# Optimization experiments

Hardware: AMD Instinct MI355X
Metric: run time of the kernel (lower is better)

The kernel has to match this reference:

```python
import jax, jax.numpy as jnp
import numpy as np

B, C, H, W = 16, 512, 32, 32
KC = C // 8  # key_channels = 64


def setup_inputs() -> dict:
    key = jax.random.key(0)
    ks = jax.random.split(key, 6)
    s_in = 1.0 / np.sqrt(C)
    return {
        "x": jax.random.normal(ks[0], (B, C, H, W), dtype=jnp.float32),
        "Wq": jax.random.normal(ks[1], (KC, C), dtype=jnp.float32) * s_in,
        "bq": jnp.zeros((KC,), dtype=jnp.float32),
        "Wk": jax.random.normal(ks[2], (KC, C), dtype=jnp.float32) * s_in,
        "bk": jnp.zeros((KC,), dtype=jnp.float32),
        "Wv": jax.random.normal(ks[3], (C, C), dtype=jnp.float32) * s_in,
        "bv": jnp.zeros((C,), dtype=jnp.float32),
        "Wo": jax.random.normal(ks[4], (C, C), dtype=jnp.float32) * s_in,
        "bo": jnp.zeros((C,), dtype=jnp.float32),
        "gamma": jnp.zeros((1,), dtype=jnp.float32),
    }


def reference(x, Wq, bq, Wk, bk, Wv, bv, Wo, bo, gamma):
    b, c, h, w = x.shape
    n = h * w
    kc = Wq.shape[0]
    xf = x.reshape(b, c, n)  # [B, C, N]
    # 1x1 convs == channel matmuls
    q = jnp.einsum('kc,bcn->bnk', Wq, xf) + bq  # [B, N, KC]
    k = jnp.einsum('kc,bcn->bkn', Wk, xf) + bk[None, :, None]  # [B, KC, N]
    v = jnp.einsum('vc,bcn->bnv', Wv, xf) + bv  # [B, N, C]
    scale = jnp.asarray(kc, x.dtype) ** -0.5
    att = jax.nn.softmax(jnp.einsum('bnk,bkm->bnm', q, k) * scale, axis=-1)  # [B, N, N]
    out = jnp.einsum('bnm,bmv->bnv', att, v)  # [B, N, C]
    out = jnp.einsum('cv,bnv->bcn', Wo, out) + bo[None, :, None]  # [B, C, N]
    out = gamma[0] * out + xf
    return out.reshape(b, c, h, w)
```

## Files before the change

kernel.cpp:

```cpp
#include <hip/hip_runtime.h>
#include <cstddef>


typedef unsigned short ushort_t;
typedef __attribute__((ext_vector_type(8))) short bf16x8;
typedef __attribute__((ext_vector_type(4))) float f32x4;

#define QSCALE 0.18033688011112042f

__device__ __forceinline__ ushort_t f2bf_t(float f) {
  return (ushort_t)(__float_as_uint(f) >> 16);
}
__device__ __forceinline__ unsigned pk2bf(float lo, float hi) {
  return __builtin_amdgcn_perm(__float_as_uint(hi), __float_as_uint(lo),
                               0x07060302u);
}

__device__ __forceinline__ void gload16(const ushort_t* g, ushort_t* l) {
  __builtin_amdgcn_global_load_lds(
      (const __attribute__((address_space(1))) void*)g,
      (__attribute__((address_space(3))) void*)l, 16, 0, 0);
}

template <int TM>
__device__ __forceinline__ void gemm_core(
    const ushort_t* __restrict__ A, int lda,
    const ushort_t* __restrict__ B, int ldb,
    int K, int m0, int n0,
    ushort_t* As, ushort_t* Bs, f32x4 (*acc)[4])
{
  constexpr int MT  = TM / 32;
  constexpr int WTM = TM / 2;
  const int t = threadIdx.x;
  const int lane = t & 63, quad = lane >> 4, l15 = lane & 15;
  const int w = t >> 6, wm = w >> 1, wn = w & 1;
  const int rr = (lane >> 3) & 7;
  const int gg = (lane & 7) ^ rr;

  #pragma unroll
  for (int i = 0; i < MT; ++i)
    #pragma unroll
    for (int j = 0; j < 4; ++j) acc[i][j] = (f32x4){0.f, 0.f, 0.f, 0.f};

  for (int k0 = 0; k0 < K; k0 += 64) {
    #pragma unroll
    for (int i = 0; i < TM / 32; ++i) {
      const int mrow = w * (TM / 4) + i * 8;
      gload16(A + (size_t)(m0 + mrow + rr) * lda + k0 + gg * 8, As + mrow * 64);
    }
    #pragma unroll
    for (int i = 0; i < 4; ++i) {
      const int mrow = w * 32 + i * 8;
      gload16(B + (size_t)(n0 + mrow + rr) * ldb + k0 + gg * 8, Bs + mrow * 64);
    }
    __syncthreads();
    #pragma unroll
    for (int kk = 0; kk < 2; ++kk) {
      const int gq = kk * 4 + quad;
      const int sg = (gq ^ (l15 & 7)) * 8;
      bf16x8 af[MT], bfr[4];
      #pragma unroll
      for (int i = 0; i < MT; ++i)
        af[i] = *(const bf16x8*)(As + (wm * WTM + i * 16 + l15) * 64 + sg);
      #pragma unroll
      for (int j = 0; j < 4; ++j)
        bfr[j] = *(const bf16x8*)(Bs + (wn * 64 + j * 16 + l15) * 64 + sg);
      #pragma unroll
      for (int i = 0; i < MT; ++i)
        #pragma unroll
        for (int j = 0; j < 4; ++j)
          acc[i][j] = __builtin_amdgcn_mfma_f32_16x16x32_bf16(
              af[i], bfr[j], acc[i][j], 0, 0, 0);
    }
    __syncthreads();
  }
}

template <int TM, class F>
__device__ __forceinline__ void store_bf16(
    ushort_t* lds, ushort_t* __restrict__ out, int ldo, int m0, int n0,
    f32x4 (*acc)[4], F f)
{
  constexpr int MT = TM / 32, WTM = TM / 2, SI = TM / 16;
  const int t = threadIdx.x;
  const int lane = t & 63, quad = lane >> 4, l15 = lane & 15;
  const int w = t >> 6, wm = w >> 1, wn = w & 1;
  #pragma unroll
  for (int i = 0; i < MT; ++i)
    #pragma unroll
    for (int j = 0; j < 4; ++j)
      #pragma unroll
      for (int r = 0; r < 4; ++r) {
        const int rl = wm * WTM + i * 16 + quad * 4 + r;
        const int cl = wn * 64 + j * 16 + l15;
        lds[rl * 136 + cl] = f2bf_t(f(i, j, r, rl, cl, acc[i][j][r]));
      }
  __syncthreads();
  #pragma unroll
  for (int i = 0; i < SI; ++i) {
    const int s = i * 256 + t, m = s >> 4, g = s & 15;
    const uint4 v = *(const uint4*)(lds + m * 136 + g * 8);
    *(uint4*)(out + (size_t)(m0 + m) * ldo + n0 + g * 8) = v;
  }
}

__global__ __launch_bounds__(256) void prep_x(
    const float* __restrict__ x,
    const float* __restrict__ Wq, const float* __restrict__ Wk,
    const float* __restrict__ Wv, const float* __restrict__ Wo,
    ushort_t* __restrict__ xbfT, ushort_t* __restrict__ Wqk,
    ushort_t* __restrict__ Wvb, ushort_t* __restrict__ Wob)
{
  __shared__ float T[64][65];
  const int t = threadIdx.x;
  if (blockIdx.y == 8) {
    const int id = blockIdx.z * 16 + blockIdx.x;
    #pragma unroll
    for (int p = 0; p < 5; ++p) {
      const int s = p * 256 + t;
      if (s < 1152) {
        const int u = id * 1152 + s;
        const int e = u * 2;
        float f0, f1;
        if (e < 32768)       { f0 = Wq[e];         f1 = Wq[e + 1]; }
        else if (e < 65536)  { f0 = Wk[e - 32768]; f1 = Wk[e - 32767]; }
        else if (e < 327680) { f0 = Wv[e - 65536]; f1 = Wv[e - 65535]; }
        else                 { f0 = Wo[e - 327680]; f1 = Wo[e - 327679]; }
        const unsigned pk = pk2bf(f0, f1);
        if (e < 65536)       *((unsigned*)Wqk + u) = pk;
        else if (e < 327680) *((unsigned*)Wvb + (u - 32768)) = pk;
        else                 *((unsigned*)Wob + (u - 163840)) = pk;
      }
    }
    return;
  }
  const int b = blockIdx.z, c0 = blockIdx.y * 64, n0 = blockIdx.x * 64;
  const float* xb = x + ((size_t)b * 512 + c0) * 1024 + n0;
  const int nj = t & 63, ci0 = t >> 6;
  #pragma unroll
  for (int p = 0; p < 16; ++p) {
    const int ci = p * 4 + ci0;
    T[ci][nj] = xb[(size_t)ci * 1024 + nj];
  }
  __syncthreads();
  const int c2 = (t & 31) * 2, nr0 = t >> 5;
  #pragma unroll
  for (int p = 0; p < 8; ++p) {
    const int nr = p * 8 + nr0;
    *(unsigned*)&xbfT[((size_t)b * 1024 + n0 + nr) * 512 + c0 + c2] =
        pk2bf(T[c2][nr], T[c2 + 1][nr]);
  }
}

__global__ __launch_bounds__(256) void k1_fused(
    const ushort_t* __restrict__ xbfT, const ushort_t* __restrict__ Wqk,
    const ushort_t* __restrict__ Wvb,
    const float* __restrict__ bq, const float* __restrict__ bk,
    const float* __restrict__ bv,
    ushort_t* __restrict__ qkt, ushort_t* __restrict__ vt2)
{
  __shared__ __align__(16) ushort_t lds[17408];
  const int bid = blockIdx.x;
  const int t = threadIdx.x, lane = t & 63, quad = lane >> 4, l15 = lane & 15;
  const int w = t >> 6, wm = w >> 1, wn = w & 1;
  if (bid < 512) {
    const int b = bid >> 5, my = (bid >> 3) & 3, nx = bid & 7;
    const int m0 = my * 128, n0 = nx * 128;
    f32x4 acc[4][4];
    gemm_core<128>(Wvb, 512, xbfT + (size_t)b * 524288, 512, 512, m0, n0,
                   lds, lds + 128 * 64, acc);
    float br[4][4];
    #pragma unroll
    for (int i = 0; i < 4; ++i)
      #pragma unroll
      for (int r = 0; r < 4; ++r)
        br[i][r] = bv[m0 + wm * 64 + i * 16 + quad * 4 + r];
    store_bf16<128>(lds, vt2 + (size_t)b * 524288, 1024, m0, n0, acc,
        [&](int i, int, int r, int, int, float v) { return v + br[i][r]; });
  } else {
    const int id = bid - 512, b = id >> 4, my = id & 15;
    const int m0 = my * 64;
    f32x4 acc[2][4];
    gemm_core<64>(xbfT + (size_t)b * 524288, 512, Wqk, 512, 512, m0, 0,
                  lds, lds + 64 * 64, acc);
    float bc[4], qs[4];
    #pragma unroll
    for (int j = 0; j < 4; ++j) {
      const int col = wn * 64 + j * 16 + l15;
      bc[j] = (col < 64) ? bq[col] : bk[col - 64];
      qs[j] = (col < 64) ? QSCALE : 1.0f;
    }
    store_bf16<64>(lds, qkt + (size_t)b * 131072, 128, m0, 0, acc,
        [&](int, int j, int, int, int, float v) { return (v + bc[j]) * qs[j]; });
  }
}

__global__ __launch_bounds__(256) void flash_attn(
    const ushort_t* __restrict__ qkt, const ushort_t* __restrict__ vt2,
    ushort_t* __restrict__ o1)
{
  __shared__ __align__(16) ushort_t buf[33792];
  __shared__ float lsum[64][2];
  ushort_t* Ks0 = buf;
  ushort_t* Vs0 = buf + 8192;
  ushort_t* Ps0 = buf + 24576;

  const int t = threadIdx.x;
  const int lane = t & 63, quad = lane >> 4, l15 = lane & 15;
  const int w = t >> 6, wm = w >> 1, wn = w & 1;
  const int rr = (lane >> 3) & 7, gg = (lane & 7) ^ rr;

  const unsigned lin = blockIdx.x;
  const unsigned wid = (lin & 7) * 128 + (lin >> 3);
  const int b  = wid >> 6;
  const int m0 = ((wid >> 2) & 15) * 64;
  const int c0 = (wid & 3) * 128;

  const ushort_t* qb = qkt + (size_t)b * 131072;
  const ushort_t* vb = vt2 + (size_t)b * 524288;

  #pragma unroll
  for (int i = 0; i < 2; ++i) {
    const int mrow = w * 16 + i * 8;
    gload16(qb + (size_t)(m0 + mrow + rr) * 128 + gg * 8, Ps0 + mrow * 64);
  }
  asm volatile("s_waitcnt vmcnt(0)" ::: "memory");
  __builtin_amdgcn_s_barrier();

  bf16x8 af_q[2][2];
  #pragma unroll
  for (int kk = 0; kk < 2; ++kk) {
    const int sg = ((kk * 4 + quad) ^ (l15 & 7)) * 8;
    #pragma unroll
    for (int i = 0; i < 2; ++i)
      af_q[i][kk] = *(const bf16x8*)(Ps0 + (wm * 32 + i * 16 + l15) * 64 + sg);
  }

  const ushort_t* kp = qb + (size_t)(w * 16 + rr) * 128 + 64 + gg * 8;
  const ushort_t* vp = vb + (size_t)(c0 + w * 32 + rr) * 1024 + gg * 8;

  #pragma unroll
  for (int i = 0; i < 2; ++i)
    gload16(kp + i * 1024, Ks0 + (w * 16 + i * 8) * 64);
  #pragma unroll
  for (int i = 0; i < 4; ++i)
    gload16(vp + i * 8192, Vs0 + (w * 32 + i * 8) * 64);
  asm volatile("s_waitcnt vmcnt(0) lgkmcnt(0)" ::: "memory");
  __builtin_amdgcn_s_barrier();

  f32x4 accO[2][4];
  #pragma unroll
  for (int i = 0; i < 2; ++i)
    #pragma unroll
    for (int j = 0; j < 4; ++j) accO[i][j] = (f32x4){0.f, 0.f, 0.f, 0.f};
  float rsum[2][4] = {{0.f, 0.f, 0.f, 0.f}, {0.f, 0.f, 0.f, 0.f}};

  const int psw_off = (wm * 32 + quad * 4) * 72 + wn * 32 + l15;
  const int sg0 = (quad ^ (l15 & 7)) * 8;
  const int sg1 = ((4 + quad) ^ (l15 & 7)) * 8;

  const ushort_t* kpn = kp + 8192;
  const ushort_t* vpn = vp + 64;
  int p = 0;

  #pragma unroll 1
  for (int mc = 0; mc < 1024; mc += 64) {
    ushort_t* Ksd = p ? Ks0 + 4096 : Ks0;
    ushort_t* Vsd = p ? Vs0 + 8192 : Vs0;
    ushort_t* Psd = p ? Ps0 + 4608 : Ps0;
    ushort_t* Ksn = p ? Ks0 : Ks0 + 4096;
    ushort_t* Vsn = p ? Vs0 : Vs0 + 8192;

    if (mc < 960) {
      #pragma unroll
      for (int i = 0; i < 2; ++i)
        gload16(kpn + i * 1024, Ksn + (w * 16 + i * 8) * 64);
      #pragma unroll
      for (int i = 0; i < 4; ++i)
        gload16(vpn + i * 8192, Vsn + (w * 32 + i * 8) * 64);
    }

    f32x4 accS[2][2];
    #pragma unroll
    for (int i = 0; i < 2; ++i)
      #pragma unroll
      for (int j = 0; j < 2; ++j) accS[i][j] = (f32x4){0.f, 0.f, 0.f, 0.f};
    #pragma unroll
    for (int kk = 0; kk < 2; ++kk) {
      const int sg = kk ? sg1 : sg0;
      bf16x8 bk_[2];
      #pragma unroll
      for (int j = 0; j < 2; ++j)
        bk_[j] = *(const bf16x8*)(Ksd + (wn * 32 + j * 16 + l15) * 64 + sg);
      #pragma unroll
      for (int i = 0; i < 2; ++i)
        #pragma unroll
        for (int j = 0; j < 2; ++j)
          accS[i][j] = __builtin_amdgcn_mfma_f32_16x16x32_bf16(
              af_q[i][kk], bk_[j], accS[i][j], 0, 0, 0);
    }

    ushort_t* psw = Psd + psw_off;
    #pragma unroll
    for (int i = 0; i < 2; ++i)
      #pragma unroll
      for (int j = 0; j < 2; ++j)
        #pragma unroll
        for (int r = 0; r < 4; ++r) {
          const float e = __builtin_amdgcn_exp2f(accS[i][j][r]);
          rsum[i][r] += e;
          psw[(i * 16 + r) * 72 + j * 16] = f2bf_t(e);
        }

    asm volatile("s_waitcnt lgkmcnt(0)" ::: "memory");
    __builtin_amdgcn_s_barrier();

    #pragma unroll
    for (int kk = 0; kk < 2; ++kk) {
      const int gq = kk * 4 + quad;
      const int sgv = kk ? sg1 : sg0;
      bf16x8 ap[2], bv_[4];
      #pragma unroll
      for (int i = 0; i < 2; ++i)
        ap[i] = *(const bf16x8*)(Psd + (wm * 32 + i * 16 + l15) * 72 + gq * 8);
      #pragma unroll
      for (int j = 0; j < 4; ++j)
        bv_[j] = *(const bf16x8*)(Vsd + (wn * 64 + j * 16 + l15) * 64 + sgv);
      #pragma unroll
      for (int i = 0; i < 2; ++i)
        #pragma unroll
        for (int j = 0; j < 4; ++j)
          accO[i][j] = __builtin_amdgcn_mfma_f32_16x16x32_bf16(
              ap[i], bv_[j], accO[i][j], 0, 0, 0);
    }

    asm volatile("s_waitcnt vmcnt(0)" ::: "memory");
    __builtin_amdgcn_s_barrier();

    kpn += 8192;
    vpn += 64;
    p ^= 1;
  }

  #pragma unroll
  for (int i = 0; i < 2; ++i)
    #pragma unroll
    for (int r = 0; r < 4; ++r) {
      float s = rsum[i][r];
      #pragma unroll
      for (int d = 1; d < 16; d <<= 1) s += __shfl_xor(s, d, 16);
      if (l15 == 0) lsum[wm * 32 + i * 16 + quad * 4 + r][wn] = s;
    }
  __syncthreads();

  ushort_t* fl_b = buf;
  #pragma unroll
  for (int i = 0; i < 2; ++i)
    #pragma unroll
    for (int r = 0; r < 4; ++r) {
      const int row = wm * 32 + i * 16 + quad * 4 + r;
      const float inv = 1.0f / (lsum[row][0] + lsum[row][1]);
      #pragma unroll
      for (int j = 0; j < 4; ++j)
        fl_b[row * 136 + wn * 64 + j * 16 + l15] = f2bf_t(accO[i][j][r] * inv);
    }
  __syncthreads();
  #pragma unroll
  for (int pp = 0; pp < 4; ++pp) {
    const int s = pp * 256 + t, m = s >> 4, g = s & 15;
    const uint4 v = *(const uint4*)(fl_b + m * 136 + g * 8);
    *(uint4*)(o1 + ((size_t)b * 1024 + m0 + m) * 512 + c0 + g * 8) = v;
  }
}

__global__ __launch_bounds__(256) void k4_proj(
    const ushort_t* __restrict__ Wob, const ushort_t* __restrict__ o1,
    const float* __restrict__ bo, const float* __restrict__ gamma,
    const float* __restrict__ x, float* __restrict__ out)
{
  __shared__ __align__(16) ushort_t lds[128 * 136];
  const int b = blockIdx.z, m0 = blockIdx.y * 128, n0 = blockIdx.x * 128;
  f32x4 acc[4][4];
  gemm_core<128>(Wob, 512, o1 + (size_t)b * 524288, 512, 512, m0, n0,
                 lds, lds + 128 * 64, acc);
  const int t = threadIdx.x, lane = t & 63, quad = lane >> 4, l15 = lane & 15;
  const int w = t >> 6, wm = w >> 1, wn = w & 1;
  const float g = gamma[0];
  float br[4][4];
  #pragma unroll
  for (int i = 0; i < 4; ++i)
    #pragma unroll
    for (int r = 0; r < 4; ++r)
      br[i][r] = bo[m0 + wm * 64 + i * 16 + quad * 4 + r];
  float* fl = (float*)lds;
  #pragma unroll
  for (int h = 0; h < 2; ++h) {
    if (wm == h) {
      #pragma unroll
      for (int i = 0; i < 4; ++i)
        #pragma unroll
        for (int j = 0; j < 4; ++j)
          #pragma unroll
          for (int r = 0; r < 4; ++r)
            fl[(i * 16 + quad * 4 + r) * 132 + wn * 64 + j * 16 + l15] =
                g * (acc[i][j][r] + br[i][r]);
    }
    __syncthreads();
    #pragma unroll
    for (int i2 = 0; i2 < 8; ++i2) {
      const int s = i2 * 256 + t, m = s >> 5, c4 = s & 31;
      f32x4 v = *(const f32x4*)(fl + m * 132 + c4 * 4);
      const size_t gi = ((size_t)b * 512 + m0 + h * 64 + m) * 1024 + n0 + c4 * 4;
      const f32x4 xr = *(const f32x4*)(x + gi);
      v += xr;
      *(f32x4*)(out + gi) = v;
    }
    __syncthreads();
  }
}

extern "C" void kernel_launch(void* const* d_in, const int* in_sizes, int n_in,
                              void* d_out, int out_size, void* d_ws, size_t ws_size,
                              hipStream_t stream) {
  const float* x     = (const float*)d_in[0];
  const float* Wq    = (const float*)d_in[1];
  const float* bq    = (const float*)d_in[2];
  const float* Wk    = (const float*)d_in[3];
  const float* bk    = (const float*)d_in[4];
  const float* Wv    = (const float*)d_in[5];
  const float* bv    = (const float*)d_in[6];
  const float* Wo    = (const float*)d_in[7];
  const float* bo    = (const float*)d_in[8];
  const float* gamma = (const float*)d_in[9];
  float* out = (float*)d_out;

  char* wsp = (char*)d_ws;
  ushort_t* xbfT   = (ushort_t*)wsp;  wsp += (size_t)16 * 1024 * 512 * 2;
  ushort_t* Wqk_bf = (ushort_t*)wsp;  wsp += (size_t)128 * 512 * 2;
  ushort_t* Wv_bf  = (ushort_t*)wsp;  wsp += (size_t)512 * 512 * 2;
  ushort_t* Wo_bf  = (ushort_t*)wsp;  wsp += (size_t)512 * 512 * 2;
  ushort_t* qkt    = (ushort_t*)wsp;  wsp += (size_t)16 * 1024 * 128 * 2;
  ushort_t* vt2    = (ushort_t*)wsp;  wsp += (size_t)16 * 512 * 1024 * 2;
  ushort_t* o1     = xbfT;

  prep_x    <<<dim3(16, 9, 16), 256, 0, stream>>>(x, Wq, Wk, Wv, Wo,
                                                  xbfT, Wqk_bf, Wv_bf, Wo_bf);
  k1_fused  <<<768, 256, 0, stream>>>(xbfT, Wqk_bf, Wv_bf, bq, bk, bv, qkt, vt2);
  flash_attn<<<dim3(1024), 256, 0, stream>>>(qkt, vt2, o1);
  k4_proj   <<<dim3(8, 4, 16), 256, 0, stream>>>(Wo_bf, o1, bo, gamma, x, out);
}
```

Before: 188.9 us.

## Double-buffer GEMM LDS tiles, vectorize prep transpose, remap blocks per XCD

```diff
diff --git a/kernel.cpp b/kernel.cpp
--- a/kernel.cpp
+++ b/kernel.cpp
@@ -5,6 +5,8 @@
 typedef unsigned short ushort_t;
 typedef __attribute__((ext_vector_type(8))) short bf16x8;
 typedef __attribute__((ext_vector_type(4))) float f32x4;
+typedef __attribute__((ext_vector_type(2))) float f32x2;
+typedef __attribute__((ext_vector_type(2))) unsigned u32x2;
 
 #define QSCALE 0.18033688011112042f
 
@@ -37,23 +39,35 @@
   const int rr = (lane >> 3) & 7;
   const int gg = (lane & 7) ^ rr;
 
-  #pragma unroll
-  for (int i = 0; i < MT; ++i)
-    #pragma unroll
-    for (int j = 0; j < 4; ++j) acc[i][j] = (f32x4){0.f, 0.f, 0.f, 0.f};
-
-  for (int k0 = 0; k0 < K; k0 += 64) {
+  auto stage = [&](int k0, int pbuf) {
+    ushort_t* Ad = As + pbuf * (TM * 64);
+    ushort_t* Bd = Bs + pbuf * (128 * 64);
     #pragma unroll
     for (int i = 0; i < TM / 32; ++i) {
       const int mrow = w * (TM / 4) + i * 8;
-      gload16(A + (size_t)(m0 + mrow + rr) * lda + k0 + gg * 8, As + mrow * 64);
+      gload16(A + (size_t)(m0 + mrow + rr) * lda + k0 + gg * 8, Ad + mrow * 64);
     }
     #pragma unroll
     for (int i = 0; i < 4; ++i) {
       const int mrow = w * 32 + i * 8;
-      gload16(B + (size_t)(n0 + mrow + rr) * ldb + k0 + gg * 8, Bs + mrow * 64);
-    }
-    __syncthreads();
+      gload16(B + (size_t)(n0 + mrow + rr) * ldb + k0 + gg * 8, Bd + mrow * 64);
+    }
+  };
+
+  stage(0, 0);
+
+  #pragma unroll
+  for (int i = 0; i < MT; ++i)
+    #pragma unroll
+    for (int j = 0; j < 4; ++j) acc[i][j] = (f32x4){0.f, 0.f, 0.f, 0.f};
+
+  __syncthreads();
+
+  int pb = 0;
+  for (int k0 = 0; k0 < K; k0 += 64) {
+    if (k0 + 64 < K) stage(k0 + 64, pb ^ 1);
+    const ushort_t* Ac = As + pb * (TM * 64);
+    const ushort_t* Bc = Bs + pb * (128 * 64);
     #pragma unroll
     for (int kk = 0; kk < 2; ++kk) {
       const int gq = kk * 4 + quad;
@@ -61,10 +75,10 @@
       bf16x8 af[MT], bfr[4];
       #pragma unroll
       for (int i = 0; i < MT; ++i)
-        af[i] = *(const bf16x8*)(As + (wm * WTM + i * 16 + l15) * 64 + sg);
+        af[i] = *(const bf16x8*)(Ac + (wm * WTM + i * 16 + l15) * 64 + sg);
       #pragma unroll
       for (int j = 0; j < 4; ++j)
-        bfr[j] = *(const bf16x8*)(Bs + (wn * 64 + j * 16 + l15) * 64 + sg);
+        bfr[j] = *(const bf16x8*)(Bc + (wn * 64 + j * 16 + l15) * 64 + sg);
       #pragma unroll
       for (int i = 0; i < MT; ++i)
         #pragma unroll
@@ -73,6 +87,7 @@
               af[i], bfr[j], acc[i][j], 0, 0, 0);
     }
     __syncthreads();
+    pb ^= 1;
   }
 }
 
@@ -111,7 +126,7 @@
     ushort_t* __restrict__ xbfT, ushort_t* __restrict__ Wqk,
     ushort_t* __restrict__ Wvb, ushort_t* __restrict__ Wob)
 {
-  __shared__ float T[64][65];
+  __shared__ float T[64 * 66];
   const int t = threadIdx.x;
   if (blockIdx.y == 8) {
     const int id = blockIdx.z * 16 + blockIdx.x;
@@ -136,19 +151,26 @@
   }
   const int b = blockIdx.z, c0 = blockIdx.y * 64, n0 = blockIdx.x * 64;
   const float* xb = x + ((size_t)b * 512 + c0) * 1024 + n0;
-  const int nj = t & 63, ci0 = t >> 6;
-  #pragma unroll
-  for (int p = 0; p < 16; ++p) {
-    const int ci = p * 4 + ci0;
-    T[ci][nj] = xb[(size_t)ci * 1024 + nj];
+  const int njf = t & 15, ci0 = t >> 4;
+  #pragma unroll
+  for (int p = 0; p < 4; ++p) {
+    const int ci = p * 16 + ci0;
+    const f32x4 v = *(const f32x4*)(xb + (size_t)ci * 1024 + njf * 4);
+    float* d = &T[ci * 66 + njf * 4];
+    *(f32x2*)(d)     = (f32x2){v[0], v[1]};
+    *(f32x2*)(d + 2) = (f32x2){v[2], v[3]};
   }
   __syncthreads();
-  const int c2 = (t & 31) * 2, nr0 = t >> 5;
-  #pragma unroll
-  for (int p = 0; p < 8; ++p) {
-    const int nr = p * 8 + nr0;
-    *(unsigned*)&xbfT[((size_t)b * 1024 + n0 + nr) * 512 + c0 + c2] =
-        pk2bf(T[c2][nr], T[c2 + 1][nr]);
+  const int c4 = (t & 15) * 4, nr0 = t >> 4;
+  #pragma unroll
+  for (int p = 0; p < 4; ++p) {
+    const int nr = p * 16 + nr0;
+    const float a0 = T[(c4 + 0) * 66 + nr];
+    const float a1 = T[(c4 + 1) * 66 + nr];
+    const float a2 = T[(c4 + 2) * 66 + nr];
+    const float a3 = T[(c4 + 3) * 66 + nr];
+    const u32x2 pkv = {pk2bf(a0, a1), pk2bf(a2, a3)};
+    *(u32x2*)&xbfT[((size_t)b * 1024 + n0 + nr) * 512 + c0 + c4] = pkv;
   }
 }
 
@@ -159,30 +181,30 @@
     const float* __restrict__ bv,
     ushort_t* __restrict__ qkt, ushort_t* __restrict__ vt2)
 {
-  __shared__ __align__(16) ushort_t lds[17408];
-  const int bid = blockIdx.x;
+  __shared__ __align__(16) ushort_t lds[32768];
+  const unsigned lin = blockIdx.x;
+  const unsigned wid = (lin & 7) * 96 + (lin >> 3);
+  const int b = wid / 48, r = wid % 48;
   const int t = threadIdx.x, lane = t & 63, quad = lane >> 4, l15 = lane & 15;
   const int w = t >> 6, wm = w >> 1, wn = w & 1;
-  if (bid < 512) {
-    const int b = bid >> 5, my = (bid >> 3) & 3, nx = bid & 7;
-    const int m0 = my * 128, n0 = nx * 128;
+  if (r < 32) {
+    const int m0 = (r >> 3) * 128, n0 = (r & 7) * 128;
     f32x4 acc[4][4];
     gemm_core<128>(Wvb, 512, xbfT + (size_t)b * 524288, 512, 512, m0, n0,
-                   lds, lds + 128 * 64, acc);
+                   lds, lds + 16384, acc);
     float br[4][4];
     #pragma unroll
     for (int i = 0; i < 4; ++i)
       #pragma unroll
-      for (int r = 0; r < 4; ++r)
-        br[i][r] = bv[m0 + wm * 64 + i * 16 + quad * 4 + r];
+      for (int rr2 = 0; rr2 < 4; ++rr2)
+        br[i][rr2] = bv[m0 + wm * 64 + i * 16 + quad * 4 + rr2];
     store_bf16<128>(lds, vt2 + (size_t)b * 524288, 1024, m0, n0, acc,
-        [&](int i, int, int r, int, int, float v) { return v + br[i][r]; });
+        [&](int i, int, int rr2, int, int, float v) { return v + br[i][rr2]; });
   } else {
-    const int id = bid - 512, b = id >> 4, my = id & 15;
-    const int m0 = my * 64;
+    const int m0 = (r - 32) * 64;
     f32x4 acc[2][4];
     gemm_core<64>(xbfT + (size_t)b * 524288, 512, Wqk, 512, 512, m0, 0,
-                  lds, lds + 64 * 64, acc);
+                  lds, lds + 8192, acc);
     float bc[4], qs[4];
     #pragma unroll
     for (int j = 0; j < 4; ++j) {
@@ -306,10 +328,10 @@
       #pragma unroll
       for (int j = 0; j < 2; ++j)
         #pragma unroll
-        for (int r = 0; r < 4; ++r) {
-          const float e = __builtin_amdgcn_exp2f(accS[i][j][r]);
-          rsum[i][r] += e;
-          psw[(i * 16 + r) * 72 + j * 16] = f2bf_t(e);
+        for (int r2 = 0; r2 < 4; ++r2) {
+          const float e = __builtin_amdgcn_exp2f(accS[i][j][r2]);
+          rsum[i][r2] += e;
+          psw[(i * 16 + r2) * 72 + j * 16] = f2bf_t(e);
         }
 
     asm volatile("s_waitcnt lgkmcnt(0)" ::: "memory");
@@ -345,11 +367,11 @@
   #pragma unroll
   for (int i = 0; i < 2; ++i)
     #pragma unroll
-    for (int r = 0; r < 4; ++r) {
-      float s = rsum[i][r];
+    for (int r2 = 0; r2 < 4; ++r2) {
+      float s = rsum[i][r2];
       #pragma unroll
       for (int d = 1; d < 16; d <<= 1) s += __shfl_xor(s, d, 16);
-      if (l15 == 0) lsum[wm * 32 + i * 16 + quad * 4 + r][wn] = s;
+      if (l15 == 0) lsum[wm * 32 + i * 16 + quad * 4 + r2][wn] = s;
     }
   __syncthreads();
 
@@ -357,12 +379,12 @@
   #pragma unroll
   for (int i = 0; i < 2; ++i)
     #pragma unroll
-    for (int r = 0; r < 4; ++r) {
-      const int row = wm * 32 + i * 16 + quad * 4 + r;
+    for (int r2 = 0; r2 < 4; ++r2) {
+      const int row = wm * 32 + i * 16 + quad * 4 + r2;
       const float inv = 1.0f / (lsum[row][0] + lsum[row][1]);
       #pragma unroll
       for (int j = 0; j < 4; ++j)
-        fl_b[row * 136 + wn * 64 + j * 16 + l15] = f2bf_t(accO[i][j][r] * inv);
+        fl_b[row * 136 + wn * 64 + j * 16 + l15] = f2bf_t(accO[i][j][r2] * inv);
     }
   __syncthreads();
   #pragma unroll
@@ -378,11 +400,14 @@
     const float* __restrict__ bo, const float* __restrict__ gamma,
     const float* __restrict__ x, float* __restrict__ out)
 {
-  __shared__ __align__(16) ushort_t lds[128 * 136];
-  const int b = blockIdx.z, m0 = blockIdx.y * 128, n0 = blockIdx.x * 128;
+  __shared__ __align__(16) ushort_t lds[32768];
+  const unsigned lin = blockIdx.x;
+  const unsigned wid = (lin & 7) * 64 + (lin >> 3);
+  const int b = wid >> 5, rem = wid & 31;
+  const int m0 = (rem >> 3) * 128, n0 = (rem & 7) * 128;
   f32x4 acc[4][4];
   gemm_core<128>(Wob, 512, o1 + (size_t)b * 524288, 512, 512, m0, n0,
-                 lds, lds + 128 * 64, acc);
+                 lds, lds + 16384, acc);
   const int t = threadIdx.x, lane = t & 63, quad = lane >> 4, l15 = lane & 15;
   const int w = t >> 6, wm = w >> 1, wn = w & 1;
   const float g = gamma[0];
@@ -390,8 +415,8 @@
   #pragma unroll
   for (int i = 0; i < 4; ++i)
     #pragma unroll
-    for (int r = 0; r < 4; ++r)
-      br[i][r] = bo[m0 + wm * 64 + i * 16 + quad * 4 + r];
+    for (int r2 = 0; r2 < 4; ++r2)
+      br[i][r2] = bo[m0 + wm * 64 + i * 16 + quad * 4 + r2];
   float* fl = (float*)lds;
   #pragma unroll
   for (int h = 0; h < 2; ++h) {
@@ -401,9 +426,9 @@
         #pragma unroll
         for (int j = 0; j < 4; ++j)
           #pragma unroll
-          for (int r = 0; r < 4; ++r)
-            fl[(i * 16 + quad * 4 + r) * 132 + wn * 64 + j * 16 + l15] =
-                g * (acc[i][j][r] + br[i][r]);
+          for (int r2 = 0; r2 < 4; ++r2)
+            fl[(i * 16 + quad * 4 + r2) * 132 + wn * 64 + j * 16 + l15] =
+                g * (acc[i][j][r2] + br[i][r2]);
     }
     __syncthreads();
     #pragma unroll
@@ -447,5 +472,5 @@
                                                   xbfT, Wqk_bf, Wv_bf, Wo_bf);
   k1_fused  <<<768, 256, 0, stream>>>(xbfT, Wqk_bf, Wv_bf, bq, bk, bv, qkt, vt2);
   flash_attn<<<dim3(1024), 256, 0, stream>>>(qkt, vt2, o1);
-  k4_proj   <<<dim3(8, 4, 16), 256, 0, stream>>>(Wo_bf, o1, bo, gamma, x, out);
-}
+  k4_proj   <<<512, 256, 0, stream>>>(Wo_bf, o1, bo, gamma, x, out);
+}
```

Measured after the change: 179.0 us. 5.2% less time.
